# Optimization experiments

Hardware: AMD Instinct MI355X
Metric: run time of the kernel (lower is better)

The kernel has to match this reference:

```python
import jax, jax.numpy as jnp
import numpy as np

B, H, SQ, SK, D = 2, 16, 2048, 2048, 128
SCALE = 0.20884964425119185
P_DROP = 0.125

def setup_inputs() -> dict:
    key = jax.random.key(0)
    k1, k2, k3 = jax.random.split(key, 3)
    x1 = jax.random.normal(k1, (B, H, SQ, D), dtype=jnp.float32)
    x2 = jax.random.normal(k2, (B, H, SK, D), dtype=jnp.float32)
    # inverted dropout mask: 0 with prob p, else 1/(1-p)
    keep = jax.random.uniform(k3, (B, H, SQ, SK)) >= P_DROP
    dropout_mask = keep.astype(jnp.float32) / (1.0 - P_DROP)
    return {"x1": x1, "x2": x2, "dropout_mask": dropout_mask}

def reference(x1, x2, dropout_mask):
    # scores: [B,H,Sq,Sk]
    scores = jnp.einsum('bhqd,bhkd->bhqk', x1, x2) * SCALE
    attn = jax.nn.softmax(scores, axis=-1)
    attn = attn * dropout_mask
    # output: [B,H,Sq,D]
    return jnp.einsum('bhqk,bhkd->bhqd', attn, x2)
```

## Files before the change

kernel.cpp:

```cpp
#include <hip/hip_runtime.h>
#include <hip/hip_bf16.h>

#define SQ 2048
#define SK 2048
#define DD 128
#define NBH 32
#define QBLK 128
#define KBLK 32
#define NKT (SK / KBLK)
#define SCALE 0.20884964425119185f
#define SCL2 (SCALE * 1.4426950408889634f)

typedef __attribute__((ext_vector_type(8))) short short8;
typedef __attribute__((ext_vector_type(4))) float f32x4;

#define KPITCH 272
#define VPITCH 80
#define VOFF 8704
#define SMEM_BYTES 18944

static __device__ __forceinline__ unsigned int pk_bf16(float lo, float hi) {
    float2 f2; f2.x = lo; f2.y = hi;
    __hip_bfloat162 h = __float22bfloat162_rn(f2);
    union { __hip_bfloat162 h2; unsigned int u; } cv; cv.h2 = h;
    return cv.u;
}

#define SOFTMAX_PACK(PA, SA_, SB_, MCa, MCb, LPART)                            \
  { float p_[8];                                                               \
    p_[0] = __builtin_amdgcn_exp2f(SA_[0]*SCL2);                               \
    p_[1] = __builtin_amdgcn_exp2f(SA_[1]*SCL2);                               \
    p_[2] = __builtin_amdgcn_exp2f(SA_[2]*SCL2);                               \
    p_[3] = __builtin_amdgcn_exp2f(SA_[3]*SCL2);                               \
    p_[4] = __builtin_amdgcn_exp2f(SB_[0]*SCL2);                               \
    p_[5] = __builtin_amdgcn_exp2f(SB_[1]*SCL2);                               \
    p_[6] = __builtin_amdgcn_exp2f(SB_[2]*SCL2);                               \
    p_[7] = __builtin_amdgcn_exp2f(SB_[3]*SCL2);                               \
    LPART += ((p_[0]+p_[1]) + (p_[2]+p_[3])) + ((p_[4]+p_[5]) + (p_[6]+p_[7]));\
    p_[0]*=MCa.x; p_[1]*=MCa.y; p_[2]*=MCa.z; p_[3]*=MCa.w;                    \
    p_[4]*=MCb.x; p_[5]*=MCb.y; p_[6]*=MCb.z; p_[7]*=MCb.w;                    \
    unsigned int P0 = pk_bf16(p_[0],p_[1]), P1 = pk_bf16(p_[2],p_[3]);         \
    unsigned int P2 = pk_bf16(p_[4],p_[5]), P3 = pk_bf16(p_[6],p_[7]);         \
    unsigned int a0 = __shfl((int)P0, sA), a2 = __shfl((int)P2, sA);           \
    unsigned int b0 = __shfl((int)P1, sA), b2 = __shfl((int)P3, sA);           \
    unsigned int c0 = __shfl((int)P0, sB), c2 = __shfl((int)P2, sB);           \
    unsigned int d0 = __shfl((int)P1, sB), d2 = __shfl((int)P3, sB);           \
    union { unsigned int u[4]; short8 v; } pb_;                                \
    pb_.u[0] = hi ? a2 : a0; pb_.u[1] = hi ? b2 : b0;                          \
    pb_.u[2] = hi ? c2 : c0; pb_.u[3] = hi ? d2 : d0;                          \
    PA = pb_.v; }

#define SYNC_STAGE()                                                           \
    asm volatile("s_waitcnt lgkmcnt(0)" ::: "memory");                         \
    __builtin_amdgcn_sched_barrier(0);                                         \
    __builtin_amdgcn_s_barrier();                                              \
    __builtin_amdgcn_sched_barrier(0);

#define COMPUTE_TILE(MC0, MC1, MC2, MC3)                                       \
    f32x4 s00={0,0,0,0}, s01={0,0,0,0}, s10={0,0,0,0}, s11={0,0,0,0};          \
    __builtin_amdgcn_s_setprio(1);                                             \
    _Pragma("unroll")                                                          \
    for (int ks = 0; ks < 4; ++ks) {                                           \
      short8 ka0 = *(const short8*)(smem + (c)      * KPITCH + ks*64 + 16*g);  \
      short8 ka1 = *(const short8*)(smem + (16 + c) * KPITCH + ks*64 + 16*g);  \
      s00 = __builtin_amdgcn_mfma_f32_16x16x32_bf16(ka0, qf0[ks], s00, 0,0,0); \
      s01 = __builtin_amdgcn_mfma_f32_16x16x32_bf16(ka1, qf0[ks], s01, 0,0,0); \
      s10 = __builtin_amdgcn_mfma_f32_16x16x32_bf16(ka0, qf1[ks], s10, 0,0,0); \
      s11 = __builtin_amdgcn_mfma_f32_16x16x32_bf16(ka1, qf1[ks], s11, 0,0,0); \
    }                                                                          \
    __builtin_amdgcn_s_setprio(0);                                             \
    short8 pa0, pa1;                                                           \
    SOFTMAX_PACK(pa0, s00, s01, MC0, MC1, l0p)                                 \
    SOFTMAX_PACK(pa1, s10, s11, MC2, MC3, l1p)                                 \
    __builtin_amdgcn_s_setprio(1);                                             \
    _Pragma("unroll")                                                          \
    for (int d8 = 0; d8 < 8; ++d8) {                                           \
      short8 vv = *(const short8*)(smem + VOFF + (d8*16 + c)*VPITCH + 16*g);   \
      o0[d8] = __builtin_amdgcn_mfma_f32_16x16x32_bf16(pa0, vv, o0[d8], 0,0,0);\
      o1[d8] = __builtin_amdgcn_mfma_f32_16x16x32_bf16(pa1, vv, o1[d8], 0,0,0);\
    }                                                                          \
    __builtin_amdgcn_s_setprio(0);                                             \
    SYNC_STAGE()

#define BODY_BF(KC0, KC1, VC0, VC1, MC0, MC1, MC2, MC3,                        \
                KN0, KN1, VN0, VN1, MN0, MN1, MN2, MN3, KT)                    \
  { const int kbn = ((KT) < NKT - 1) ? ((KT) + 1) * KBLK : (KT) * KBLK;        \
    KN0 = *(const short8*)(x2bb + (size_t)(kbn + kk)      * DD + kd0);         \
    KN1 = *(const short8*)(x2bb + (size_t)(kbn + kk + 16) * DD + kd0);         \
    VN0 = *(const short8*)(x2bb + (size_t)(kbn + vk) * DD + vd0);              \
    VN1 = *(const short8*)(x2bb + (size_t)(kbn + vk) * DD + vd0 + 64);         \
    MN0 = *(const float4*)(mq0 + kbn);                                         \
    MN1 = *(const float4*)(mq0 + kbn + 16);                                    \
    MN2 = *(const float4*)(mq1 + kbn);                                         \
    MN3 = *(const float4*)(mq1 + kbn + 16);                                    \
    *(short8*)(smem + (kk)      * KPITCH + 2*kd0) = KC0;                       \
    *(short8*)(smem + (kk + 16) * KPITCH + 2*kd0) = KC1;                       \
    { union { short8 s; unsigned short u[8]; } va_, vb_;                       \
      va_.s = VC0; vb_.s = VC1;                                                \
      _Pragma("unroll")                                                        \
      for (int j = 0; j < 8; ++j) {                                            \
        *(unsigned short*)(smem + VOFF + (vd0 + j)      * VPITCH + 2*vk) = va_.u[j]; \
        *(unsigned short*)(smem + VOFF + (vd0 + 64 + j) * VPITCH + 2*vk) = vb_.u[j]; \
      } }                                                                      \
    SYNC_STAGE()                                                               \
    COMPUTE_TILE(MC0, MC1, MC2, MC3)                                           \
  }

#define BODY_F32(KC0a,KC0b,KC1a,KC1b, VC0a,VC0b,VC1a,VC1b, MC0,MC1,MC2,MC3,    \
                 KN0a,KN0b,KN1a,KN1b, VN0a,VN0b,VN1a,VN1b, MN0,MN1,MN2,MN3, KT)\
  { const int kbn = ((KT) < NKT - 1) ? ((KT) + 1) * KBLK : (KT) * KBLK;        \
    KN0a = *(const float4*)(x2fb + (size_t)(kbn + kk)      * DD + kd0);        \
    KN0b = *(const float4*)(x2fb + (size_t)(kbn + kk)      * DD + kd0 + 4);    \
    KN1a = *(const float4*)(x2fb + (size_t)(kbn + kk + 16) * DD + kd0);        \
    KN1b = *(const float4*)(x2fb + (size_t)(kbn + kk + 16) * DD + kd0 + 4);    \
    VN0a = *(const float4*)(x2fb + (size_t)(kbn + vk) * DD + vd0);             \
    VN0b = *(const float4*)(x2fb + (size_t)(kbn + vk) * DD + vd0 + 4);         \
    VN1a = *(const float4*)(x2fb + (size_t)(kbn + vk) * DD + vd0 + 64);        \
    VN1b = *(const float4*)(x2fb + (size_t)(kbn + vk) * DD + vd0 + 68);        \
    MN0 = *(const float4*)(mq0 + kbn);                                         \
    MN1 = *(const float4*)(mq0 + kbn + 16);                                    \
    MN2 = *(const float4*)(mq1 + kbn);                                         \
    MN3 = *(const float4*)(mq1 + kbn + 16);                                    \
    { union { unsigned int u[4]; short8 s; } k0_, k1_;                         \
      k0_.u[0]=pk_bf16(KC0a.x,KC0a.y); k0_.u[1]=pk_bf16(KC0a.z,KC0a.w);        \
      k0_.u[2]=pk_bf16(KC0b.x,KC0b.y); k0_.u[3]=pk_bf16(KC0b.z,KC0b.w);        \
      k1_.u[0]=pk_bf16(KC1a.x,KC1a.y); k1_.u[1]=pk_bf16(KC1a.z,KC1a.w);        \
      k1_.u[2]=pk_bf16(KC1b.x,KC1b.y); k1_.u[3]=pk_bf16(KC1b.z,KC1b.w);        \
      *(short8*)(smem + (kk)      * KPITCH + 2*kd0) = k0_.s;                   \
      *(short8*)(smem + (kk + 16) * KPITCH + 2*kd0) = k1_.s; }                 \
    { unsigned int w;                                                          \
      w = pk_bf16(VC0a.x, VC0a.y);                                             \
      *(unsigned short*)(smem + VOFF + (vd0+0)*VPITCH + 2*vk) = (unsigned short)w;       \
      *(unsigned short*)(smem + VOFF + (vd0+1)*VPITCH + 2*vk) = (unsigned short)(w>>16); \
      w = pk_bf16(VC0a.z, VC0a.w);                                             \
      *(unsigned short*)(smem + VOFF + (vd0+2)*VPITCH + 2*vk) = (unsigned short)w;       \
      *(unsigned short*)(smem + VOFF + (vd0+3)*VPITCH + 2*vk) = (unsigned short)(w>>16); \
      w = pk_bf16(VC0b.x, VC0b.y);                                             \
      *(unsigned short*)(smem + VOFF + (vd0+4)*VPITCH + 2*vk) = (unsigned short)w;       \
      *(unsigned short*)(smem + VOFF + (vd0+5)*VPITCH + 2*vk) = (unsigned short)(w>>16); \
      w = pk_bf16(VC0b.z, VC0b.w);                                             \
      *(unsigned short*)(smem + VOFF + (vd0+6)*VPITCH + 2*vk) = (unsigned short)w;       \
      *(unsigned short*)(smem + VOFF + (vd0+7)*VPITCH + 2*vk) = (unsigned short)(w>>16); \
      w = pk_bf16(VC1a.x, VC1a.y);                                             \
      *(unsigned short*)(smem + VOFF + (vd0+64)*VPITCH + 2*vk) = (unsigned short)w;      \
      *(unsigned short*)(smem + VOFF + (vd0+65)*VPITCH + 2*vk) = (unsigned short)(w>>16);\
      w = pk_bf16(VC1a.z, VC1a.w);                                             \
      *(unsigned short*)(smem + VOFF + (vd0+66)*VPITCH + 2*vk) = (unsigned short)w;      \
      *(unsigned short*)(smem + VOFF + (vd0+67)*VPITCH + 2*vk) = (unsigned short)(w>>16);\
      w = pk_bf16(VC1b.x, VC1b.y);                                             \
      *(unsigned short*)(smem + VOFF + (vd0+68)*VPITCH + 2*vk) = (unsigned short)w;      \
      *(unsigned short*)(smem + VOFF + (vd0+69)*VPITCH + 2*vk) = (unsigned short)(w>>16);\
      w = pk_bf16(VC1b.z, VC1b.w);                                             \
      *(unsigned short*)(smem + VOFF + (vd0+70)*VPITCH + 2*vk) = (unsigned short)w;      \
      *(unsigned short*)(smem + VOFF + (vd0+71)*VPITCH + 2*vk) = (unsigned short)(w>>16);\
    }                                                                          \
    SYNC_STAGE()                                                               \
    COMPUTE_TILE(MC0, MC1, MC2, MC3)                                           \
  }

#define KERNEL_PRE()                                                           \
    __shared__ __align__(16) unsigned char smem[SMEM_BYTES];                   \
    const int tid  = threadIdx.x;                                              \
    const int lane = tid & 63, wid = tid >> 6;                                 \
    const int c = lane & 15, g = lane >> 4;                                    \
    const int bid = blockIdx.x;                                                \
    const int swz = (bid & 7) * 64 + (bid >> 3);   \
    const int bh = swz >> 4;                                                   \
    const int qb = swz & 15;                                                   \
    const float* x1b = x1 + ((size_t)bh * SQ + (size_t)qb * QBLK) * DD;        \
    const float* mb  = mask + ((size_t)bh * SQ + (size_t)qb * QBLK) * SK;      \
    float*      outb = out + ((size_t)bh * SQ + (size_t)qb * QBLK) * DD;       \
    const int sA = c + ((g & 1) << 5);                                         \
    const int sB = sA + 16;                                                    \
    const bool hi = (g >= 2);                                                  \
    const int kk  = tid >> 4, kd0 = (tid & 15) * 8;                            \
    const int vk  = tid & 31, vd0 = (tid >> 5) * 8;                            \
    const float* mq0 = mb + (size_t)(wid*16 + c) * SK + 4*g;                   \
    const float* mq1 = mq0 + (size_t)64 * SK;

#define KERNEL_QLOAD()                                                         \
    short8 qf0[4], qf1[4];                                                     \
    {  const float* q0r = x1b + (size_t)(wid*16 + c) * DD;                     \
       const float* q1r = q0r + (size_t)64 * DD;                               \
       _Pragma("unroll")                                                       \
       for (int ks = 0; ks < 4; ++ks) {                                        \
           float4 a = *(const float4*)(q0r + ks*32 + 8*g);                     \
           float4 b = *(const float4*)(q0r + ks*32 + 8*g + 4);                 \
           union { unsigned int u[4]; short8 s; } t;                           \
           t.u[0]=pk_bf16(a.x,a.y); t.u[1]=pk_bf16(a.z,a.w);                   \
           t.u[2]=pk_bf16(b.x,b.y); t.u[3]=pk_bf16(b.z,b.w);                   \
           qf0[ks]=t.s;                                                        \
           a = *(const float4*)(q1r + ks*32 + 8*g);                            \
           b = *(const float4*)(q1r + ks*32 + 8*g + 4);                        \
           t.u[0]=pk_bf16(a.x,a.y); t.u[1]=pk_bf16(a.z,a.w);                   \
           t.u[2]=pk_bf16(b.x,b.y); t.u[3]=pk_bf16(b.z,b.w);                   \
           qf1[ks]=t.s;                                                        \
       } }

#define KERNEL_EPILOGUE()                                                      \
    float l0 = l0p; l0 += __shfl_xor(l0, 16); l0 += __shfl_xor(l0, 32);        \
    float l1 = l1p; l1 += __shfl_xor(l1, 16); l1 += __shfl_xor(l1, 32);        \
    float il00 = 1.0f/__shfl(l0, 4*g+0), il01 = 1.0f/__shfl(l0, 4*g+1);        \
    float il02 = 1.0f/__shfl(l0, 4*g+2), il03 = 1.0f/__shfl(l0, 4*g+3);        \
    float il10 = 1.0f/__shfl(l1, 4*g+0), il11 = 1.0f/__shfl(l1, 4*g+1);        \
    float il12 = 1.0f/__shfl(l1, 4*g+2), il13 = 1.0f/__shfl(l1, 4*g+3);        \
    float* orow0 = outb + (size_t)(wid*16) * DD;                               \
    float* orow1 = outb + (size_t)(64 + wid*16) * DD;                          \
    _Pragma("unroll")                                                          \
    for (int d8 = 0; d8 < 8; ++d8) {                                           \
        orow0[(4*g + 0) * DD + d8*16 + c] = o0[d8][0] * il00;                  \
        orow0[(4*g + 1) * DD + d8*16 + c] = o0[d8][1] * il01;                  \
        orow0[(4*g + 2) * DD + d8*16 + c] = o0[d8][2] * il02;                  \
        orow0[(4*g + 3) * DD + d8*16 + c] = o0[d8][3] * il03;                  \
        orow1[(4*g + 0) * DD + d8*16 + c] = o1[d8][0] * il10;                  \
        orow1[(4*g + 1) * DD + d8*16 + c] = o1[d8][1] * il11;                  \
        orow1[(4*g + 2) * DD + d8*16 + c] = o1[d8][2] * il12;                  \
        orow1[(4*g + 3) * DD + d8*16 + c] = o1[d8][3] * il13;                  \
    }

__global__ __launch_bounds__(256) void cvt_x2(const float* __restrict__ src,
                                              unsigned short* __restrict__ dst,
                                              int n4) {
    int i = blockIdx.x * 256 + threadIdx.x;
    const int stride = gridDim.x * 256;
    for (; i < n4; i += stride) {
        float4 v = ((const float4*)src)[i];
        uint2 w; w.x = pk_bf16(v.x, v.y); w.y = pk_bf16(v.z, v.w);
        ((uint2*)dst)[i] = w;
    }
}

__global__ __launch_bounds__(256, 2) void fattn_bf16(
    const float* __restrict__ x1, const unsigned short* __restrict__ x2b,
    const float* __restrict__ mask, float* __restrict__ out)
{
    KERNEL_PRE()
    const unsigned short* x2bb = x2b + (size_t)bh * SK * DD;

    short8 kA0 = *(const short8*)(x2bb + (size_t)(kk)      * DD + kd0);
    short8 kA1 = *(const short8*)(x2bb + (size_t)(kk + 16) * DD + kd0);
    short8 vA0 = *(const short8*)(x2bb + (size_t)(vk) * DD + vd0);
    short8 vA1 = *(const short8*)(x2bb + (size_t)(vk) * DD + vd0 + 64);
    float4 mA0 = *(const float4*)(mq0);
    float4 mA1 = *(const float4*)(mq0 + 16);
    float4 mA2 = *(const float4*)(mq1);
    float4 mA3 = *(const float4*)(mq1 + 16);
    short8 kB0, kB1, vB0, vB1; float4 mB0, mB1, mB2, mB3;

    KERNEL_QLOAD()

    f32x4 o0[8] = {}, o1[8] = {};
    float l0p = 0.f, l1p = 0.f;

    for (int kt2 = 0; kt2 < NKT / 2; ++kt2) {
        BODY_BF(kA0,kA1,vA0,vA1, mA0,mA1,mA2,mA3,
                kB0,kB1,vB0,vB1, mB0,mB1,mB2,mB3, 2*kt2)
        BODY_BF(kB0,kB1,vB0,vB1, mB0,mB1,mB2,mB3,
                kA0,kA1,vA0,vA1, mA0,mA1,mA2,mA3, 2*kt2 + 1)
    }
    KERNEL_EPILOGUE()
}

__global__ __launch_bounds__(256, 2) void fattn_f32(
    const float* __restrict__ x1, const float* __restrict__ x2,
    const float* __restrict__ mask, float* __restrict__ out)
{
    KERNEL_PRE()
    const float* x2fb = x2 + (size_t)bh * SK * DD;

    float4 kA0a = *(const float4*)(x2fb + (size_t)(kk)      * DD + kd0);
    float4 kA0b = *(const float4*)(x2fb + (size_t)(kk)      * DD + kd0 + 4);
    float4 kA1a = *(const float4*)(x2fb + (size_t)(kk + 16) * DD + kd0);
    float4 kA1b = *(const float4*)(x2fb + (size_t)(kk + 16) * DD + kd0 + 4);
    float4 vA0a = *(const float4*)(x2fb + (size_t)(vk) * DD + vd0);
    float4 vA0b = *(const float4*)(x2fb + (size_t)(vk) * DD + vd0 + 4);
    float4 vA1a = *(const float4*)(x2fb + (size_t)(vk) * DD + vd0 + 64);
    float4 vA1b = *(const float4*)(x2fb + (size_t)(vk) * DD + vd0 + 68);
    float4 mA0 = *(const float4*)(mq0);
    float4 mA1 = *(const float4*)(mq0 + 16);
    float4 mA2 = *(const float4*)(mq1);
    float4 mA3 = *(const float4*)(mq1 + 16);
    float4 kB0a,kB0b,kB1a,kB1b, vB0a,vB0b,vB1a,vB1b, mB0,mB1,mB2,mB3;

    KERNEL_QLOAD()

    f32x4 o0[8] = {}, o1[8] = {};
    float l0p = 0.f, l1p = 0.f;

    for (int kt2 = 0; kt2 < NKT / 2; ++kt2) {
        BODY_F32(kA0a,kA0b,kA1a,kA1b, vA0a,vA0b,vA1a,vA1b, mA0,mA1,mA2,mA3,
                 kB0a,kB0b,kB1a,kB1b, vB0a,vB0b,vB1a,vB1b, mB0,mB1,mB2,mB3, 2*kt2)
        BODY_F32(kB0a,kB0b,kB1a,kB1b, vB0a,vB0b,vB1a,vB1b, mB0,mB1,mB2,mB3,
                 kA0a,kA0b,kA1a,kA1b, vA0a,vA0b,vA1a,vA1b, mA0,mA1,mA2,mA3, 2*kt2+1)
    }
    KERNEL_EPILOGUE()
}

extern "C" void kernel_launch(void* const* d_in, const int* in_sizes, int n_in,
                              void* d_out, int out_size, void* d_ws, size_t ws_size,
                              hipStream_t stream) {
    const float* x1   = (const float*)d_in[0];
    const float* x2   = (const float*)d_in[1];
    const float* mask = (const float*)d_in[2];
    float* out = (float*)d_out;
    const size_t need = (size_t)NBH * SK * DD * sizeof(unsigned short);
    if (ws_size >= need) {
        unsigned short* x2b = (unsigned short*)d_ws;
        cvt_x2<<<dim3(2048), dim3(256), 0, stream>>>(x2, x2b, NBH*SK*DD/4);
        fattn_bf16<<<dim3(NBH * (SQ / QBLK)), dim3(256), 0, stream>>>(x1, x2b, mask, out);
    } else {
        fattn_f32<<<dim3(NBH * (SQ / QBLK)), dim3(256), 0, stream>>>(x1, x2, mask, out);
    }
}
```

Baseline: 206.0 us.

## Double-buffer K/V shared tiles and pack V transpose stores as 32-bit words

Splits shared memory into two K and V buffers that alternate between even and odd tiles. This removes the second barrier after each compute tile, so the next tile's stores can overlap with other waves still reading the current buffer. It also remaps V loading so each thread reads two adjacent key rows and writes packed 32-bit pairs into the transposed V tile instead of 16-bit scalar stores, halving the LDS store count. Shared memory use doubles to about 37 KB per block, which may limit occupancy.

```diff
diff --git a/kernel.cpp b/kernel.cpp
--- a/kernel.cpp
+++ b/kernel.cpp
@@ -16,8 +16,11 @@
 
 #define KPITCH 272
 #define VPITCH 80
-#define VOFF 8704
-#define SMEM_BYTES 18944
+#define K0OFF 0
+#define K1OFF 8704
+#define V0OFF 17408
+#define V1OFF 27648
+#define SMEM_BYTES 37888
 
 static __device__ __forceinline__ unsigned int pk_bf16(float lo, float hi) {
     float2 f2; f2.x = lo; f2.y = hi;
@@ -50,19 +53,19 @@
     pb_.u[2] = hi ? c2 : c0; pb_.u[3] = hi ? d2 : d0;                          \
     PA = pb_.v; }
 
-#define SYNC_STAGE()                                                           \
+#define STAGE_SYNC()                                                           \
     asm volatile("s_waitcnt lgkmcnt(0)" ::: "memory");                         \
     __builtin_amdgcn_sched_barrier(0);                                         \
-    __builtin_amdgcn_s_barrier();                                              \
+    __builtin_amdgcn_s_barrier();                 \
     __builtin_amdgcn_sched_barrier(0);
 
-#define COMPUTE_TILE(MC0, MC1, MC2, MC3)                                       \
+#define COMPUTE_TILE(KOFF_, VOFF_, MC0, MC1, MC2, MC3)                         \
     f32x4 s00={0,0,0,0}, s01={0,0,0,0}, s10={0,0,0,0}, s11={0,0,0,0};          \
     __builtin_amdgcn_s_setprio(1);                                             \
     _Pragma("unroll")                                                          \
     for (int ks = 0; ks < 4; ++ks) {                                           \
-      short8 ka0 = *(const short8*)(smem + (c)      * KPITCH + ks*64 + 16*g);  \
-      short8 ka1 = *(const short8*)(smem + (16 + c) * KPITCH + ks*64 + 16*g);  \
+      short8 ka0 = *(const short8*)(smem + (KOFF_) + (c)      * KPITCH + ks*64 + 16*g); \
+      short8 ka1 = *(const short8*)(smem + (KOFF_) + (16 + c) * KPITCH + ks*64 + 16*g); \
       s00 = __builtin_amdgcn_mfma_f32_16x16x32_bf16(ka0, qf0[ks], s00, 0,0,0); \
       s01 = __builtin_amdgcn_mfma_f32_16x16x32_bf16(ka1, qf0[ks], s01, 0,0,0); \
       s10 = __builtin_amdgcn_mfma_f32_16x16x32_bf16(ka0, qf1[ks], s10, 0,0,0); \
@@ -75,87 +78,71 @@
     __builtin_amdgcn_s_setprio(1);                                             \
     _Pragma("unroll")                                                          \
     for (int d8 = 0; d8 < 8; ++d8) {                                           \
-      short8 vv = *(const short8*)(smem + VOFF + (d8*16 + c)*VPITCH + 16*g);   \
+      short8 vv = *(const short8*)(smem + (VOFF_) + (d8*16 + c)*VPITCH + 16*g);\
       o0[d8] = __builtin_amdgcn_mfma_f32_16x16x32_bf16(pa0, vv, o0[d8], 0,0,0);\
       o1[d8] = __builtin_amdgcn_mfma_f32_16x16x32_bf16(pa1, vv, o1[d8], 0,0,0);\
     }                                                                          \
-    __builtin_amdgcn_s_setprio(0);                                             \
-    SYNC_STAGE()
-
-#define BODY_BF(KC0, KC1, VC0, VC1, MC0, MC1, MC2, MC3,                        \
-                KN0, KN1, VN0, VN1, MN0, MN1, MN2, MN3, KT)                    \
+    __builtin_amdgcn_s_setprio(0);
+
+#define BODY_BF(KC0,KC1,VC0,VC1, MC0,MC1,MC2,MC3,                              \
+                KN0,KN1,VN0,VN1, MN0,MN1,MN2,MN3, KOFF_, VOFF_, KT)            \
   { const int kbn = ((KT) < NKT - 1) ? ((KT) + 1) * KBLK : (KT) * KBLK;        \
     KN0 = *(const short8*)(x2bb + (size_t)(kbn + kk)      * DD + kd0);         \
     KN1 = *(const short8*)(x2bb + (size_t)(kbn + kk + 16) * DD + kd0);         \
-    VN0 = *(const short8*)(x2bb + (size_t)(kbn + vk) * DD + vd0);              \
-    VN1 = *(const short8*)(x2bb + (size_t)(kbn + vk) * DD + vd0 + 64);         \
+    VN0 = *(const short8*)(x2bb + (size_t)(kbn + 2*kp)     * DD + vdb);        \
+    VN1 = *(const short8*)(x2bb + (size_t)(kbn + 2*kp + 1) * DD + vdb);        \
     MN0 = *(const float4*)(mq0 + kbn);                                         \
     MN1 = *(const float4*)(mq0 + kbn + 16);                                    \
     MN2 = *(const float4*)(mq1 + kbn);                                         \
     MN3 = *(const float4*)(mq1 + kbn + 16);                                    \
-    *(short8*)(smem + (kk)      * KPITCH + 2*kd0) = KC0;                       \
-    *(short8*)(smem + (kk + 16) * KPITCH + 2*kd0) = KC1;                       \
-    { union { short8 s; unsigned short u[8]; } va_, vb_;                       \
-      va_.s = VC0; vb_.s = VC1;                                                \
+    *(short8*)(smem + (KOFF_) + (kk)      * KPITCH + 2*kd0) = KC0;             \
+    *(short8*)(smem + (KOFF_) + (kk + 16) * KPITCH + 2*kd0) = KC1;             \
+    { union { short8 s; unsigned int u[4]; } a_, b_;                           \
+      a_.s = VC0; b_.s = VC1;                                                  \
       _Pragma("unroll")                                                        \
       for (int j = 0; j < 8; ++j) {                                            \
-        *(unsigned short*)(smem + VOFF + (vd0 + j)      * VPITCH + 2*vk) = va_.u[j]; \
-        *(unsigned short*)(smem + VOFF + (vd0 + 64 + j) * VPITCH + 2*vk) = vb_.u[j]; \
+        unsigned int w = (j & 1)                                               \
+            ? ((a_.u[j>>1] >> 16) | (b_.u[j>>1] & 0xffff0000u))                \
+            : ((a_.u[j>>1] & 0xffffu) | (b_.u[j>>1] << 16));                   \
+        *(unsigned int*)(smem + (VOFF_) + (vdb + j) * VPITCH + 4*kp) = w;      \
       } }                                                                      \
-    SYNC_STAGE()                                                               \
-    COMPUTE_TILE(MC0, MC1, MC2, MC3)                                           \
+    STAGE_SYNC()                                                               \
+    COMPUTE_TILE(KOFF_, VOFF_, MC0, MC1, MC2, MC3)                             \
   }
 
-#define BODY_F32(KC0a,KC0b,KC1a,KC1b, VC0a,VC0b,VC1a,VC1b, MC0,MC1,MC2,MC3,    \
-                 KN0a,KN0b,KN1a,KN1b, VN0a,VN0b,VN1a,VN1b, MN0,MN1,MN2,MN3, KT)\
+#define BODY_F32(KC0,KC1,KC2,KC3, VC0,VC1,VC2,VC3, MC0,MC1,MC2,MC3,            \
+                 KN0,KN1,KN2,KN3, VN0,VN1,VN2,VN3, MN0,MN1,MN2,MN3,            \
+                 KOFF_, VOFF_, KT)                                             \
   { const int kbn = ((KT) < NKT - 1) ? ((KT) + 1) * KBLK : (KT) * KBLK;        \
-    KN0a = *(const float4*)(x2fb + (size_t)(kbn + kk)      * DD + kd0);        \
-    KN0b = *(const float4*)(x2fb + (size_t)(kbn + kk)      * DD + kd0 + 4);    \
-    KN1a = *(const float4*)(x2fb + (size_t)(kbn + kk + 16) * DD + kd0);        \
-    KN1b = *(const float4*)(x2fb + (size_t)(kbn + kk + 16) * DD + kd0 + 4);    \
-    VN0a = *(const float4*)(x2fb + (size_t)(kbn + vk) * DD + vd0);             \
-    VN0b = *(const float4*)(x2fb + (size_t)(kbn + vk) * DD + vd0 + 4);         \
-    VN1a = *(const float4*)(x2fb + (size_t)(kbn + vk) * DD + vd0 + 64);        \
-    VN1b = *(const float4*)(x2fb + (size_t)(kbn + vk) * DD + vd0 + 68);        \
+    KN0 = *(const float4*)(x2fb + (size_t)(kbn + kk)      * DD + kd0);         \
+    KN1 = *(const float4*)(x2fb + (size_t)(kbn + kk)      * DD + kd0 + 4);     \
+    KN2 = *(const float4*)(x2fb + (size_t)(kbn + kk + 16) * DD + kd0);         \
+    KN3 = *(const float4*)(x2fb + (size_t)(kbn + kk + 16) * DD + kd0 + 4);     \
+    VN0 = *(const float4*)(x2fb + (size_t)(kbn + 2*kp)     * DD + vdb);        \
+    VN1 = *(const float4*)(x2fb + (size_t)(kbn + 2*kp)     * DD + vdb + 4);    \
+    VN2 = *(const float4*)(x2fb + (size_t)(kbn + 2*kp + 1) * DD + vdb);        \
+    VN3 = *(const float4*)(x2fb + (size_t)(kbn + 2*kp + 1) * DD + vdb + 4);    \
     MN0 = *(const float4*)(mq0 + kbn);                                         \
     MN1 = *(const float4*)(mq0 + kbn + 16);                                    \
     MN2 = *(const float4*)(mq1 + kbn);                                         \
     MN3 = *(const float4*)(mq1 + kbn + 16);                                    \
     { union { unsigned int u[4]; short8 s; } k0_, k1_;                         \
-      k0_.u[0]=pk_bf16(KC0a.x,KC0a.y); k0_.u[1]=pk_bf16(KC0a.z,KC0a.w);        \
-      k0_.u[2]=pk_bf16(KC0b.x,KC0b.y); k0_.u[3]=pk_bf16(KC0b.z,KC0b.w);        \
-      k1_.u[0]=pk_bf16(KC1a.x,KC1a.y); k1_.u[1]=pk_bf16(KC1a.z,KC1a.w);        \
-      k1_.u[2]=pk_bf16(KC1b.x,KC1b.y); k1_.u[3]=pk_bf16(KC1b.z,KC1b.w);        \
-      *(short8*)(smem + (kk)      * KPITCH + 2*kd0) = k0_.s;                   \
-      *(short8*)(smem + (kk + 16) * KPITCH + 2*kd0) = k1_.s; }                 \
-    { unsigned int w;                                                          \
-      w = pk_bf16(VC0a.x, VC0a.y);                                             \
-      *(unsigned short*)(smem + VOFF + (vd0+0)*VPITCH + 2*vk) = (unsigned short)w;       \
-      *(unsigned short*)(smem + VOFF + (vd0+1)*VPITCH + 2*vk) = (unsigned short)(w>>16); \
-      w = pk_bf16(VC0a.z, VC0a.w);                                             \
-      *(unsigned short*)(smem + VOFF + (vd0+2)*VPITCH + 2*vk) = (unsigned short)w;       \
-      *(unsigned short*)(smem + VOFF + (vd0+3)*VPITCH + 2*vk) = (unsigned short)(w>>16); \
-      w = pk_bf16(VC0b.x, VC0b.y);                                             \
-      *(unsigned short*)(smem + VOFF + (vd0+4)*VPITCH + 2*vk) = (unsigned short)w;       \
-      *(unsigned short*)(smem + VOFF + (vd0+5)*VPITCH + 2*vk) = (unsigned short)(w>>16); \
-      w = pk_bf16(VC0b.z, VC0b.w);                                             \
-      *(unsigned short*)(smem + VOFF + (vd0+6)*VPITCH + 2*vk) = (unsigned short)w;       \
-      *(unsigned short*)(smem + VOFF + (vd0+7)*VPITCH + 2*vk) = (unsigned short)(w>>16); \
-      w = pk_bf16(VC1a.x, VC1a.y);                                             \
-      *(unsigned short*)(smem + VOFF + (vd0+64)*VPITCH + 2*vk) = (unsigned short)w;      \
-      *(unsigned short*)(smem + VOFF + (vd0+65)*VPITCH + 2*vk) = (unsigned short)(w>>16);\
-      w = pk_bf16(VC1a.z, VC1a.w);                                             \
-      *(unsigned short*)(smem + VOFF + (vd0+66)*VPITCH + 2*vk) = (unsigned short)w;      \
-      *(unsigned short*)(smem + VOFF + (vd0+67)*VPITCH + 2*vk) = (unsigned short)(w>>16);\
-      w = pk_bf16(VC1b.x, VC1b.y);                                             \
-      *(unsigned short*)(smem + VOFF + (vd0+68)*VPITCH + 2*vk) = (unsigned short)w;      \
-      *(unsigned short*)(smem + VOFF + (vd0+69)*VPITCH + 2*vk) = (unsigned short)(w>>16);\
-      w = pk_bf16(VC1b.z, VC1b.w);                                             \
-      *(unsigned short*)(smem + VOFF + (vd0+70)*VPITCH + 2*vk) = (unsigned short)w;      \
-      *(unsigned short*)(smem + VOFF + (vd0+71)*VPITCH + 2*vk) = (unsigned short)(w>>16);\
-    }                                                                          \
-    SYNC_STAGE()                                                               \
-    COMPUTE_TILE(MC0, MC1, MC2, MC3)                                           \
+      k0_.u[0]=pk_bf16(KC0.x,KC0.y); k0_.u[1]=pk_bf16(KC0.z,KC0.w);            \
+      k0_.u[2]=pk_bf16(KC1.x,KC1.y); k0_.u[3]=pk_bf16(KC1.z,KC1.w);            \
+      k1_.u[0]=pk_bf16(KC2.x,KC2.y); k1_.u[1]=pk_bf16(KC2.z,KC2.w);            \
+      k1_.u[2]=pk_bf16(KC3.x,KC3.y); k1_.u[3]=pk_bf16(KC3.z,KC3.w);            \
+      *(short8*)(smem + (KOFF_) + (kk)      * KPITCH + 2*kd0) = k0_.s;         \
+      *(short8*)(smem + (KOFF_) + (kk + 16) * KPITCH + 2*kd0) = k1_.s; }       \
+    *(unsigned int*)(smem + (VOFF_) + (vdb+0)*VPITCH + 4*kp) = pk_bf16(VC0.x, VC2.x); \
+    *(unsigned int*)(smem + (VOFF_) + (vdb+1)*VPITCH + 4*kp) = pk_bf16(VC0.y, VC2.y); \
+    *(unsigned int*)(smem + (VOFF_) + (vdb+2)*VPITCH + 4*kp) = pk_bf16(VC0.z, VC2.z); \
+    *(unsigned int*)(smem + (VOFF_) + (vdb+3)*VPITCH + 4*kp) = pk_bf16(VC0.w, VC2.w); \
+    *(unsigned int*)(smem + (VOFF_) + (vdb+4)*VPITCH + 4*kp) = pk_bf16(VC1.x, VC3.x); \
+    *(unsigned int*)(smem + (VOFF_) + (vdb+5)*VPITCH + 4*kp) = pk_bf16(VC1.y, VC3.y); \
+    *(unsigned int*)(smem + (VOFF_) + (vdb+6)*VPITCH + 4*kp) = pk_bf16(VC1.z, VC3.z); \
+    *(unsigned int*)(smem + (VOFF_) + (vdb+7)*VPITCH + 4*kp) = pk_bf16(VC1.w, VC3.w); \
+    STAGE_SYNC()                                                               \
+    COMPUTE_TILE(KOFF_, VOFF_, MC0, MC1, MC2, MC3)                             \
   }
 
 #define KERNEL_PRE()                                                           \
@@ -174,7 +161,7 @@
     const int sB = sA + 16;                                                    \
     const bool hi = (g >= 2);                                                  \
     const int kk  = tid >> 4, kd0 = (tid & 15) * 8;                            \
-    const int vk  = tid & 31, vd0 = (tid >> 5) * 8;                            \
+    const int kp  = tid & 15, vdb = (tid >> 4) * 8;                            \
     const float* mq0 = mb + (size_t)(wid*16 + c) * SK + 4*g;                   \
     const float* mq1 = mq0 + (size_t)64 * SK;
 
@@ -239,8 +226,8 @@
 
     short8 kA0 = *(const short8*)(x2bb + (size_t)(kk)      * DD + kd0);
     short8 kA1 = *(const short8*)(x2bb + (size_t)(kk + 16) * DD + kd0);
-    short8 vA0 = *(const short8*)(x2bb + (size_t)(vk) * DD + vd0);
-    short8 vA1 = *(const short8*)(x2bb + (size_t)(vk) * DD + vd0 + 64);
+    short8 vA0 = *(const short8*)(x2bb + (size_t)(2*kp)     * DD + vdb);
+    short8 vA1 = *(const short8*)(x2bb + (size_t)(2*kp + 1) * DD + vdb);
     float4 mA0 = *(const float4*)(mq0);
     float4 mA1 = *(const float4*)(mq0 + 16);
     float4 mA2 = *(const float4*)(mq1);
@@ -254,9 +241,9 @@
 
     for (int kt2 = 0; kt2 < NKT / 2; ++kt2) {
         BODY_BF(kA0,kA1,vA0,vA1, mA0,mA1,mA2,mA3,
-                kB0,kB1,vB0,vB1, mB0,mB1,mB2,mB3, 2*kt2)
+                kB0,kB1,vB0,vB1, mB0,mB1,mB2,mB3, K0OFF, V0OFF, 2*kt2)
         BODY_BF(kB0,kB1,vB0,vB1, mB0,mB1,mB2,mB3,
-                kA0,kA1,vA0,vA1, mA0,mA1,mA2,mA3, 2*kt2 + 1)
+                kA0,kA1,vA0,vA1, mA0,mA1,mA2,mA3, K1OFF, V1OFF, 2*kt2 + 1)
     }
     KERNEL_EPILOGUE()
 }
@@ -268,19 +255,19 @@
     KERNEL_PRE()
     const float* x2fb = x2 + (size_t)bh * SK * DD;
 
-    float4 kA0a = *(const float4*)(x2fb + (size_t)(kk)      * DD + kd0);
-    float4 kA0b = *(const float4*)(x2fb + (size_t)(kk)      * DD + kd0 + 4);
-    float4 kA1a = *(const float4*)(x2fb + (size_t)(kk + 16) * DD + kd0);
-    float4 kA1b = *(const float4*)(x2fb + (size_t)(kk + 16) * DD + kd0 + 4);
-    float4 vA0a = *(const float4*)(x2fb + (size_t)(vk) * DD + vd0);
-    float4 vA0b = *(const float4*)(x2fb + (size_t)(vk) * DD + vd0 + 4);
-    float4 vA1a = *(const float4*)(x2fb + (size_t)(vk) * DD + vd0 + 64);
-    float4 vA1b = *(const float4*)(x2fb + (size_t)(vk) * DD + vd0 + 68);
+    float4 kA0 = *(const float4*)(x2fb + (size_t)(kk)      * DD + kd0);
+    float4 kA1 = *(const float4*)(x2fb + (size_t)(kk)      * DD + kd0 + 4);
+    float4 kA2 = *(const float4*)(x2fb + (size_t)(kk + 16) * DD + kd0);
+    float4 kA3 = *(const float4*)(x2fb + (size_t)(kk + 16) * DD + kd0 + 4);
+    float4 vA0 = *(const float4*)(x2fb + (size_t)(2*kp)     * DD + vdb);
+    float4 vA1 = *(const float4*)(x2fb + (size_t)(2*kp)     * DD + vdb + 4);
+    float4 vA2 = *(const float4*)(x2fb + (size_t)(2*kp + 1) * DD + vdb);
+    float4 vA3 = *(const float4*)(x2fb + (size_t)(2*kp + 1) * DD + vdb + 4);
     float4 mA0 = *(const float4*)(mq0);
     float4 mA1 = *(const float4*)(mq0 + 16);
     float4 mA2 = *(const float4*)(mq1);
     float4 mA3 = *(const float4*)(mq1 + 16);
-    float4 kB0a,kB0b,kB1a,kB1b, vB0a,vB0b,vB1a,vB1b, mB0,mB1,mB2,mB3;
+    float4 kB0,kB1,kB2,kB3, vB0,vB1,vB2,vB3, mB0,mB1,mB2,mB3;
 
     KERNEL_QLOAD()
 
@@ -288,10 +275,12 @@
     float l0p = 0.f, l1p = 0.f;
 
     for (int kt2 = 0; kt2 < NKT / 2; ++kt2) {
-        BODY_F32(kA0a,kA0b,kA1a,kA1b, vA0a,vA0b,vA1a,vA1b, mA0,mA1,mA2,mA3,
-                 kB0a,kB0b,kB1a,kB1b, vB0a,vB0b,vB1a,vB1b, mB0,mB1,mB2,mB3, 2*kt2)
-        BODY_F32(kB0a,kB0b,kB1a,kB1b, vB0a,vB0b,vB1a,vB1b, mB0,mB1,mB2,mB3,
-                 kA0a,kA0b,kA1a,kA1b, vA0a,vA0b,vA1a,vA1b, mA0,mA1,mA2,mA3, 2*kt2+1)
+        BODY_F32(kA0,kA1,kA2,kA3, vA0,vA1,vA2,vA3, mA0,mA1,mA2,mA3,
+                 kB0,kB1,kB2,kB3, vB0,vB1,vB2,vB3, mB0,mB1,mB2,mB3,
+                 K0OFF, V0OFF, 2*kt2)
+        BODY_F32(kB0,kB1,kB2,kB3, vB0,vB1,vB2,vB3, mB0,mB1,mB2,mB3,
+                 kA0,kA1,kA2,kA3, vA0,vA1,vA2,vA3, mA0,mA1,mA2,mA3,
+                 K1OFF, V1OFF, 2*kt2 + 1)
     }
     KERNEL_EPILOGUE()
 }
```

After: 223.2 us. 1.08x slower.
